# Performance work log

Measured on AMD Instinct MI355X. Metric: run time of the kernel, lower is better.

The kernel has to match this reference:

```python
import jax, jax.numpy as jnp
import numpy as np
from jax import lax

SIZE = 64
N_SUPPORT = 8192
N_QUERIES = 16384
UNROLLING_STEPS = 10


def setup_inputs() -> dict:
    key = jax.random.key(0)
    ks = jax.random.split(key, 6)
    s = 1.0 / np.sqrt(SIZE)
    return {
        "support": jax.random.normal(ks[0], (N_SUPPORT, SIZE), jnp.float32),
        "queries": jax.random.normal(ks[1], (N_QUERIES, SIZE), jnp.float32),
        "W_ih": jax.random.normal(ks[2], (4 * SIZE, SIZE), jnp.float32) * s,
        "W_hh": jax.random.normal(ks[3], (4 * SIZE, SIZE), jnp.float32) * s,
        "b_ih": jax.random.normal(ks[4], (4 * SIZE,), jnp.float32) * s,
        "b_hh": jax.random.normal(ks[5], (4 * SIZE,), jnp.float32) * s,
    }


def _lstm_cell(x, h, c, W_ih, W_hh, b_ih, b_hh):
    # PyTorch LSTMCell gate order: i, f, g, o
    gates = x @ W_ih.T + b_ih + h @ W_hh.T + b_hh  # [B, 4*size]
    i, f, g, o = jnp.split(gates, 4, axis=1)
    c_new = jax.nn.sigmoid(f) * c + jax.nn.sigmoid(i) * jnp.tanh(g)
    h_new = jax.nn.sigmoid(o) * jnp.tanh(c_new)
    return h_new, c_new


def reference(support, queries, W_ih, W_hh, b_ih, b_hh):
    def step(carry, _):
        h_hat, c = carry
        h = h_hat + queries                              # [B, size]
        att = jax.nn.softmax(h @ support.T, axis=1)      # [B, n_support]
        readout = att @ support                          # [B, size]
        h_hat2, c2 = _lstm_cell(queries, h + readout, c, W_ih, W_hh, b_ih, b_hh)
        return (h_hat2, c2), None

    init = (jnp.zeros_like(queries), jnp.zeros_like(queries))
    (h_hat, _), _ = lax.scan(step, init, None, length=UNROLLING_STEPS)
    return h_hat + queries
```

## Files before the change

### kernel.cpp

```cpp
#include <hip/hip_runtime.h>

using u16 = unsigned short;
using u32 = unsigned int;

#define NS 8192
#define NQ 16384
#define SZ 64
#define STEPS 10
#define TS 64
#define TSZ (TS * SZ)
#define NT (NS / TS)
#define NR (NT / 2)
#define L2E 1.44269504088896340736f

typedef __attribute__((ext_vector_type(8))) _Float16 f16x8;
typedef __attribute__((ext_vector_type(4))) float f32x4;

static __device__ __forceinline__ float ex2(float x) { float r; asm("v_exp_f32 %0, %1" : "=v"(r) : "v"(x)); return r; }
static __device__ __forceinline__ float rcp_(float x) { float r; asm("v_rcp_f32 %0, %1" : "=v"(r) : "v"(x)); return r; }

static __device__ __forceinline__ u16 hbits(_Float16 h) { union { _Float16 h; u16 u; } c; c.h = h; return c.u; }
static __device__ __forceinline__ u32 pk2(float lo, float hi) {
    return (u32)hbits((_Float16)lo) | ((u32)hbits((_Float16)hi) << 16);
}
static __device__ __forceinline__ f32x4 MMH(f16x8 a, f16x8 b, f32x4 c) {
    return __builtin_amdgcn_mfma_f32_16x16x32_f16(a, b, c, 0, 0, 0);
}
static __device__ __forceinline__ f16x8 LD(const void* p) { return *(const f16x8*)p; }
static __device__ __forceinline__ float sig(float x) { return rcp_(1.f + ex2(-L2E * x)); }
static __device__ __forceinline__ float tanh_(float x) {
    float e = ex2(-2.f * L2E * x);
    return (1.f - e) * rcp_(1.f + e);
}
static __device__ __forceinline__ void lds_fence() {
    asm volatile("s_waitcnt lgkmcnt(0)" ::: "memory");
    __builtin_amdgcn_sched_barrier(0);
}
static __device__ __forceinline__ void gload16(const void* g, void* l) {
    __builtin_amdgcn_global_load_lds(
        (const __attribute__((address_space(1))) void*)g,
        (__attribute__((address_space(3))) void*)l, 16, 0, 0);
}

__global__ void prep_kernel(const float* __restrict__ sup,
                            const float* __restrict__ Wih,
                            const float* __restrict__ Whh,
                            const float* __restrict__ bih,
                            const float* __restrict__ bhh,
                            u16* __restrict__ supH, u16* __restrict__ supL,
                            u16* __restrict__ supT,
                            u16* __restrict__ WiH, u16* __restrict__ WiL,
                            u16* __restrict__ WhH, u16* __restrict__ WhL,
                            float* __restrict__ bs) {
    int i = blockIdx.x * 256 + threadIdx.x;
    if (i < NS * SZ) {
        float v = sup[i];
        _Float16 hi = (_Float16)v;
        _Float16 lo = (_Float16)(v - (float)hi);
        supH[i] = hbits(hi);
        supL[i] = hbits(lo);
        int s = i >> 6, d = i & 63;
        supT[(s >> 6) * TSZ + d * TS + (s & 63)] = hbits(hi);
    }
    if (i < 4 * SZ * SZ) {
        float a = Wih[i]; _Float16 ah = (_Float16)a;
        WiH[i] = hbits(ah); WiL[i] = hbits((_Float16)(a - (float)ah));
        float b = Whh[i]; _Float16 bh = (_Float16)b;
        WhH[i] = hbits(bh); WhL[i] = hbits((_Float16)(b - (float)bh));
    }
    if (i < 4 * SZ) bs[i] = bih[i] + bhh[i];
}

__global__ __launch_bounds__(1024, 4) void attlstm_kernel(
    const float* __restrict__ queries,
    const u16* __restrict__ supH, const u16* __restrict__ supL,
    const u16* __restrict__ supT,
    const u16* __restrict__ WiH, const u16* __restrict__ WiL,
    const u16* __restrict__ WhH, const u16* __restrict__ WhL,
    const float* __restrict__ bsum,
    float* __restrict__ out) {
    __shared__ __align__(16) u16 stage[4][3][TSZ];
    __shared__ __align__(16) u32 P_lds[16][512];
    __shared__ __align__(16) u16 hsl[4][2048];
    __shared__ __align__(16) float bs_lds[256];

    const int tid = threadIdx.x;
    const int w = tid >> 6;
    const int l = tid & 63;
    const int qg = w & 3;
    const int quarter = w >> 2;
    const int tsel = quarter >> 1;
    const int shalf = quarter & 1;
    const bool lead = (quarter == 0);
    const int q = l & 15;
    const int g = l >> 4;
    const int qrow = blockIdx.x * 64 + qg * 16 + q;
    const u32 swz = (u32)(q & 7) << 4;

    if (tid < 256) bs_lds[tid] = bsum[tid];

    const u16* gsrc[3]; int inoff[3]; int ctsel[3];
#pragma unroll
    for (int j = 0; j < 3; ++j) {
        int c = w + 16 * j;
        ctsel[j] = c / 24;
        int rem = c - 24 * ctsel[j];
        int a = rem >> 3, s8 = rem & 7;
        int srcoff = (s8 * 8 + (l >> 3)) * SZ + ((l & 7) ^ (l >> 3)) * 8;
        gsrc[j] = ((a == 0) ? supH : (a == 1) ? supL : supT) + srcoff;
        inoff[j] = a * TSZ + s8 * 512;
    }
    u16* stg = &stage[0][0][0];
    char* hslb = (char*)&hsl[qg][0];
    char* pw = (char*)&P_lds[w][0];

    float qv[16], hh[16], cc[16];
    f16x8 qfh0, qfh1, qfl0, qfl1;
    if (lead) {
#pragma unroll
        for (int s4 = 0; s4 < 4; ++s4) {
            f32x4 v = *(const f32x4*)&queries[qrow * SZ + 16 * s4 + 4 * g];
#pragma unroll
            for (int jj = 0; jj < 4; ++jj) {
                qv[4 * s4 + jj] = v[jj];
                hh[4 * s4 + jj] = 0.f;
                cc[4 * s4 + jj] = 0.f;
            }
            _Float16 c0 = (_Float16)v[0], c1 = (_Float16)v[1], c2 = (_Float16)v[2], c3 = (_Float16)v[3];
            uint2 whi, wlo;
            whi.x = (u32)hbits(c0) | ((u32)hbits(c1) << 16);
            whi.y = (u32)hbits(c2) | ((u32)hbits(c3) << 16);
            wlo.x = pk2(v[0] - (float)c0, v[1] - (float)c1);
            wlo.y = pk2(v[2] - (float)c2, v[3] - (float)c3);
            u32 b = q * 128 + ((32u * s4 + 8u * g) ^ swz);
            *(uint2*)(hslb + b) = whi;
            *(uint2*)(hslb + 2048 + b) = wlo;
        }
        lds_fence();
        qfh0 = LD(hslb + q * 128 + ((16u * g) ^ swz));
        qfh1 = LD(hslb + q * 128 + ((16u * g + 64u) ^ swz));
        qfl0 = LD(hslb + 2048 + q * 128 + ((16u * g) ^ swz));
        qfl1 = LD(hslb + 2048 + q * 128 + ((16u * g + 64u) ^ swz));
    }

#pragma unroll 1
    for (int step = 0; step < STEPS; ++step) {
        if (lead) {
#pragma unroll
            for (int s4 = 0; s4 < 4; ++s4) {
                float h0 = hh[4 * s4 + 0] + qv[4 * s4 + 0];
                float h1 = hh[4 * s4 + 1] + qv[4 * s4 + 1];
                float h2 = hh[4 * s4 + 2] + qv[4 * s4 + 2];
                float h3 = hh[4 * s4 + 3] + qv[4 * s4 + 3];
                _Float16 a0 = (_Float16)h0, a1 = (_Float16)h1, a2 = (_Float16)h2, a3 = (_Float16)h3;
                uint2 whi, wlo;
                whi.x = (u32)hbits(a0) | ((u32)hbits(a1) << 16);
                whi.y = (u32)hbits(a2) | ((u32)hbits(a3) << 16);
                wlo.x = pk2(h0 - (float)a0, h1 - (float)a1);
                wlo.y = pk2(h2 - (float)a2, h3 - (float)a3);
                u32 b = q * 128 + ((32u * s4 + 8u * g) ^ swz);
                *(uint2*)(hslb + b) = whi;
                *(uint2*)(hslb + 2048 + b) = wlo;
            }
        }
        __syncthreads();
        const f16x8 bh0 = LD(hslb + q * 128 + ((16u * g) ^ swz));
        const f16x8 bh1 = LD(hslb + q * 128 + ((16u * g + 64u) ^ swz));
        const f16x8 bl0 = LD(hslb + 2048 + q * 128 + ((16u * g) ^ swz));
        const f16x8 bl1 = LD(hslb + 2048 + q * 128 + ((16u * g + 64u) ^ swz));

#pragma unroll
        for (int j = 0; j < 3; ++j)
            gload16(gsrc[j] + ctsel[j] * TSZ, stg + ctsel[j] * 12288 + inoff[j]);
        __syncthreads();

        float m = -1e30f, mL = -1.5e30f, lsum = 0.f;
        f32x4 Oa[4] = {{0, 0, 0, 0}, {0, 0, 0, 0}, {0, 0, 0, 0}, {0, 0, 0, 0}};

#pragma unroll 1
        for (int r = 0; r < NR; ++r) {
            if (r < NR - 1) {
#pragma unroll
                for (int j = 0; j < 3; ++j) {
                    int t = 2 * r + 2 + ctsel[j];
                    gload16(gsrc[j] + t * TSZ, stg + (t & 3) * 12288 + inoff[j]);
                }
            }
            const int myslot = (2 * r + tsel) & 3;
            const char* sH = (const char*)(stg + myslot * 12288);
            const char* sL = sH + TSZ * 2;
            const char* sT = sH + 2 * TSZ * 2;
            f32x4 sv[2];
#pragma unroll
            for (int sub = 0; sub < 2; ++sub) {
                u32 rb = (u32)(16 * (2 * shalf + sub) + q) * 128;
                f16x8 aH0 = LD(sH + rb + ((16u * g) ^ swz));
                f16x8 aH1 = LD(sH + rb + ((16u * g + 64u) ^ swz));
                f16x8 aL0 = LD(sL + rb + ((16u * g) ^ swz));
                f16x8 aL1 = LD(sL + rb + ((16u * g + 64u) ^ swz));
                f32x4 a = {0, 0, 0, 0};
                a = MMH(aH0, bh0, a); a = MMH(aH1, bh1, a);
                a = MMH(aH0, bl0, a); a = MMH(aH1, bl1, a);
                a = MMH(aL0, bh0, a); a = MMH(aL1, bh1, a);
                sv[sub] = a;
            }
            float tm = fmaxf(fmaxf(fmaxf(sv[0][0], sv[0][1]), fmaxf(sv[0][2], sv[0][3])),
                             fmaxf(fmaxf(sv[1][0], sv[1][1]), fmaxf(sv[1][2], sv[1][3])));
            tm = fmaxf(tm, __shfl_xor(tm, 16));
            tm = fmaxf(tm, __shfl_xor(tm, 32));
            if (__any(tm > m + 5.5f)) {
                float mn = fmaxf(m, tm);
                float sc = ex2((m - mn) * L2E);
                lsum *= sc;
                Oa[0] *= sc; Oa[1] *= sc; Oa[2] *= sc; Oa[3] *= sc;
                m = mn; mL = m * L2E;
            }
#pragma unroll
            for (int sub = 0; sub < 2; ++sub) {
                float p0 = ex2(sv[sub][0] * L2E - mL);
                float p1 = ex2(sv[sub][1] * L2E - mL);
                float p2 = ex2(sv[sub][2] * L2E - mL);
                float p3 = ex2(sv[sub][3] * L2E - mL);
                lsum += (p0 + p1) + (p2 + p3);
                uint2 wv; wv.x = pk2(p0, p1); wv.y = pk2(p2, p3);
                *(uint2*)(pw + q * 128 + ((32u * sub + 8u * g) ^ swz)) = wv;
            }
            lds_fence();
            f16x8 pb = LD(pw + q * 128 + ((16u * g) ^ swz));
            u32 kbT = (16u * g + 64u * shalf) ^ swz;
#pragma unroll
            for (int dsub = 0; dsub < 4; ++dsub) {
                f16x8 aT = LD(sT + (u32)(16 * dsub + q) * 128 + kbT);
                Oa[dsub] = MMH(aT, pb, Oa[dsub]);
            }
            __syncthreads();
        }
        lsum += __shfl_xor(lsum, 16);
        lsum += __shfl_xor(lsum, 32);

        float* mg = (float*)stg;
        float* mine = mg + (u32)(w * 64 + l) * 20;
        *(f32x4*)(mine + 0) = Oa[0];
        *(f32x4*)(mine + 4) = Oa[1];
        *(f32x4*)(mine + 8) = Oa[2];
        *(f32x4*)(mine + 12) = Oa[3];
        mine[16] = m; mine[17] = lsum;
        __syncthreads();

        if (lead) {
#pragma unroll
            for (int k = 1; k < 4; ++k) {
                const float* oth = mg + (u32)((w + 4 * k) * 64 + l) * 20;
                f32x4 Ob0 = *(const f32x4*)(oth + 0);
                f32x4 Ob1 = *(const f32x4*)(oth + 4);
                f32x4 Ob2 = *(const f32x4*)(oth + 8);
                f32x4 Ob3 = *(const f32x4*)(oth + 12);
                float mo = oth[16], lo_ = oth[17];
                float M = fmaxf(m, mo);
                float sA = ex2((m - M) * L2E), sB = ex2((mo - M) * L2E);
                lsum = lsum * sA + lo_ * sB;
                Oa[0] = Oa[0] * sA + Ob0 * sB;
                Oa[1] = Oa[1] * sA + Ob1 * sB;
                Oa[2] = Oa[2] * sA + Ob2 * sB;
                Oa[3] = Oa[3] * sA + Ob3 * sB;
                m = M;
            }
            float inv = rcp_(lsum);

#pragma unroll
            for (int s4 = 0; s4 < 4; ++s4) {
                float r0 = hh[4 * s4 + 0] + qv[4 * s4 + 0] + Oa[s4][0] * inv;
                float r1 = hh[4 * s4 + 1] + qv[4 * s4 + 1] + Oa[s4][1] * inv;
                float r2 = hh[4 * s4 + 2] + qv[4 * s4 + 2] + Oa[s4][2] * inv;
                float r3 = hh[4 * s4 + 3] + qv[4 * s4 + 3] + Oa[s4][3] * inv;
                _Float16 a0 = (_Float16)r0, a1 = (_Float16)r1, a2 = (_Float16)r2, a3 = (_Float16)r3;
                uint2 whi, wlo;
                whi.x = (u32)hbits(a0) | ((u32)hbits(a1) << 16);
                whi.y = (u32)hbits(a2) | ((u32)hbits(a3) << 16);
                wlo.x = pk2(r0 - (float)a0, r1 - (float)a1);
                wlo.y = pk2(r2 - (float)a2, r3 - (float)a3);
                u32 b = q * 128 + ((32u * s4 + 8u * g) ^ swz);
                *(uint2*)(hslb + b) = whi;
                *(uint2*)(hslb + 2048 + b) = wlo;
            }
            lds_fence();
            const f16x8 rh0 = LD(hslb + q * 128 + ((16u * g) ^ swz));
            const f16x8 rh1 = LD(hslb + q * 128 + ((16u * g + 64u) ^ swz));
            const f16x8 rl0 = LD(hslb + 2048 + q * 128 + ((16u * g) ^ swz));
            const f16x8 rl1 = LD(hslb + 2048 + q * 128 + ((16u * g + 64u) ^ swz));

#pragma unroll
            for (int s4 = 0; s4 < 4; ++s4) {
                f32x4 ga[4];
#pragma unroll
                for (int ch = 0; ch < 4; ++ch) {
                    int u_ = 4 * ch + s4;
                    f32x4 a = *(const f32x4*)&bs_lds[16 * u_ + 4 * g];
                    const u16* wiH = WiH + (16 * u_ + q) * SZ + 8 * g;
                    const u16* wiL = WiL + (16 * u_ + q) * SZ + 8 * g;
                    const u16* whH = WhH + (16 * u_ + q) * SZ + 8 * g;
                    const u16* whL = WhL + (16 * u_ + q) * SZ + 8 * g;
                    f16x8 w0 = LD(wiH), w1 = LD(wiH + 32);
                    a = MMH(w0, qfh0, a); a = MMH(w1, qfh1, a);
                    a = MMH(w0, qfl0, a); a = MMH(w1, qfl1, a);
                    a = MMH(LD(wiL), qfh0, a); a = MMH(LD(wiL + 32), qfh1, a);
                    f16x8 v0 = LD(whH), v1 = LD(whH + 32);
                    a = MMH(v0, rh0, a); a = MMH(v1, rh1, a);
                    a = MMH(v0, rl0, a); a = MMH(v1, rl1, a);
                    a = MMH(LD(whL), rh0, a); a = MMH(LD(whL + 32), rh1, a);
                    ga[ch] = a;
                }
#pragma unroll
                for (int jj = 0; jj < 4; ++jj) {
                    int tt = 4 * s4 + jj;
                    float gi = sig(ga[0][jj]);
                    float gf = sig(ga[1][jj]);
                    float gg = tanh_(ga[2][jj]);
                    float go = sig(ga[3][jj]);
                    float cn = gf * cc[tt] + gi * gg;
                    cc[tt] = cn;
                    hh[tt] = go * tanh_(cn);
                }
            }
        }
    }

    if (lead) {
#pragma unroll
        for (int s4 = 0; s4 < 4; ++s4) {
            f32x4 v;
#pragma unroll
            for (int jj = 0; jj < 4; ++jj) v[jj] = hh[4 * s4 + jj] + qv[4 * s4 + jj];
            *(f32x4*)&out[qrow * SZ + 16 * s4 + 4 * g] = v;
        }
    }
}

extern "C" void kernel_launch(void* const* d_in, const int* in_sizes, int n_in,
                              void* d_out, int out_size, void* d_ws, size_t ws_size,
                              hipStream_t stream) {
    const float* support = (const float*)d_in[0];
    const float* queries = (const float*)d_in[1];
    const float* W_ih = (const float*)d_in[2];
    const float* W_hh = (const float*)d_in[3];
    const float* b_ih = (const float*)d_in[4];
    const float* b_hh = (const float*)d_in[5];
    float* out = (float*)d_out;

    u16* supH = (u16*)d_ws;
    u16* supL = supH + NS * SZ;
    u16* supT = supL + NS * SZ;
    u16* WiH = supT + NS * SZ;
    u16* WiL = WiH + 4 * SZ * SZ;
    u16* WhH = WiL + 4 * SZ * SZ;
    u16* WhL = WhH + 4 * SZ * SZ;
    float* bs = (float*)(WhL + 4 * SZ * SZ);

    prep_kernel<<<(NS * SZ) / 256, 256, 0, stream>>>(support, W_ih, W_hh, b_ih, b_hh,
                                                     supH, supL, supT, WiH, WiL, WhH, WhL, bs);
    attlstm_kernel<<<NQ / 64, 1024, 0, stream>>>(queries, supH, supL, supT,
                                                 WiH, WiL, WhH, WhL, bs, out);
}
```

Measured before the change: 1.460 ms.

## Distribute softmax merge and LSTM cell across all waves instead of lead waves

Before, only the 4 lead waves (quarter 0) did the cross-wave softmax merge, the h/readout conversion and the full LSTM gate matmuls while 12 waves idled. Now every wave handles one 16-column slice (its quarter) of h, c and the gates: each merges the 4 partial attention results for its slice, writes its slice to LDS, and computes one quarter of the gate MFMAs. This shrinks the serial per-step epilogue and per-thread state, at the cost of extra __syncthreads barriers. The launch_bounds occupancy hint is also dropped.

```diff
diff --git a/kernel.cpp b/kernel.cpp
--- a/kernel.cpp
+++ b/kernel.cpp
@@ -71,7 +71,7 @@
     if (i < 4 * SZ) bs[i] = bih[i] + bhh[i];
 }
 
-__global__ __launch_bounds__(1024, 4) void attlstm_kernel(
+__global__ __launch_bounds__(1024) void attlstm_kernel(
     const float* __restrict__ queries,
     const u16* __restrict__ supH, const u16* __restrict__ supL,
     const u16* __restrict__ supT,
@@ -91,11 +91,11 @@
     const int quarter = w >> 2;
     const int tsel = quarter >> 1;
     const int shalf = quarter & 1;
-    const bool lead = (quarter == 0);
     const int q = l & 15;
     const int g = l >> 4;
     const int qrow = blockIdx.x * 64 + qg * 16 + q;
     const u32 swz = (u32)(q & 7) << 4;
+    const u32 bsl = (u32)q * 128 + ((32u * (u32)quarter + 8u * (u32)g) ^ swz);
 
     if (tid < 256) bs_lds[tid] = bsum[tid];
 
@@ -114,54 +114,39 @@
     char* hslb = (char*)&hsl[qg][0];
     char* pw = (char*)&P_lds[w][0];
 
-    float qv[16], hh[16], cc[16];
-    f16x8 qfh0, qfh1, qfl0, qfl1;
-    if (lead) {
-#pragma unroll
-        for (int s4 = 0; s4 < 4; ++s4) {
-            f32x4 v = *(const f32x4*)&queries[qrow * SZ + 16 * s4 + 4 * g];
-#pragma unroll
-            for (int jj = 0; jj < 4; ++jj) {
-                qv[4 * s4 + jj] = v[jj];
-                hh[4 * s4 + jj] = 0.f;
-                cc[4 * s4 + jj] = 0.f;
-            }
-            _Float16 c0 = (_Float16)v[0], c1 = (_Float16)v[1], c2 = (_Float16)v[2], c3 = (_Float16)v[3];
-            uint2 whi, wlo;
-            whi.x = (u32)hbits(c0) | ((u32)hbits(c1) << 16);
-            whi.y = (u32)hbits(c2) | ((u32)hbits(c3) << 16);
-            wlo.x = pk2(v[0] - (float)c0, v[1] - (float)c1);
-            wlo.y = pk2(v[2] - (float)c2, v[3] - (float)c3);
-            u32 b = q * 128 + ((32u * s4 + 8u * g) ^ swz);
-            *(uint2*)(hslb + b) = whi;
-            *(uint2*)(hslb + 2048 + b) = wlo;
-        }
-        lds_fence();
-        qfh0 = LD(hslb + q * 128 + ((16u * g) ^ swz));
-        qfh1 = LD(hslb + q * 128 + ((16u * g + 64u) ^ swz));
-        qfl0 = LD(hslb + 2048 + q * 128 + ((16u * g) ^ swz));
-        qfl1 = LD(hslb + 2048 + q * 128 + ((16u * g + 64u) ^ swz));
-    }
+    float qv[4], hh[4], cc[4];
+    {
+        f32x4 v = *(const f32x4*)&queries[qrow * SZ + 16 * quarter + 4 * g];
+#pragma unroll
+        for (int jj = 0; jj < 4; ++jj) { qv[jj] = v[jj]; hh[jj] = 0.f; cc[jj] = 0.f; }
+        _Float16 c0 = (_Float16)v[0], c1 = (_Float16)v[1], c2 = (_Float16)v[2], c3 = (_Float16)v[3];
+        uint2 whi, wlo;
+        whi.x = (u32)hbits(c0) | ((u32)hbits(c1) << 16);
+        whi.y = (u32)hbits(c2) | ((u32)hbits(c3) << 16);
+        wlo.x = pk2(v[0] - (float)c0, v[1] - (float)c1);
+        wlo.y = pk2(v[2] - (float)c2, v[3] - (float)c3);
+        *(uint2*)(hslb + bsl) = whi;
+        *(uint2*)(hslb + 2048 + bsl) = wlo;
+    }
+    __syncthreads();
+    const f16x8 qfh0 = LD(hslb + q * 128 + ((16u * g) ^ swz));
+    const f16x8 qfh1 = LD(hslb + q * 128 + ((16u * g + 64u) ^ swz));
+    const f16x8 qfl0 = LD(hslb + 2048 + q * 128 + ((16u * g) ^ swz));
+    const f16x8 qfl1 = LD(hslb + 2048 + q * 128 + ((16u * g + 64u) ^ swz));
 
 #pragma unroll 1
     for (int step = 0; step < STEPS; ++step) {
-        if (lead) {
-#pragma unroll
-            for (int s4 = 0; s4 < 4; ++s4) {
-                float h0 = hh[4 * s4 + 0] + qv[4 * s4 + 0];
-                float h1 = hh[4 * s4 + 1] + qv[4 * s4 + 1];
-                float h2 = hh[4 * s4 + 2] + qv[4 * s4 + 2];
-                float h3 = hh[4 * s4 + 3] + qv[4 * s4 + 3];
-                _Float16 a0 = (_Float16)h0, a1 = (_Float16)h1, a2 = (_Float16)h2, a3 = (_Float16)h3;
-                uint2 whi, wlo;
-                whi.x = (u32)hbits(a0) | ((u32)hbits(a1) << 16);
-                whi.y = (u32)hbits(a2) | ((u32)hbits(a3) << 16);
-                wlo.x = pk2(h0 - (float)a0, h1 - (float)a1);
-                wlo.y = pk2(h2 - (float)a2, h3 - (float)a3);
-                u32 b = q * 128 + ((32u * s4 + 8u * g) ^ swz);
-                *(uint2*)(hslb + b) = whi;
-                *(uint2*)(hslb + 2048 + b) = wlo;
-            }
+        __syncthreads();
+        {
+            float h0 = hh[0] + qv[0], h1 = hh[1] + qv[1], h2 = hh[2] + qv[2], h3 = hh[3] + qv[3];
+            _Float16 a0 = (_Float16)h0, a1 = (_Float16)h1, a2 = (_Float16)h2, a3 = (_Float16)h3;
+            uint2 whi, wlo;
+            whi.x = (u32)hbits(a0) | ((u32)hbits(a1) << 16);
+            whi.y = (u32)hbits(a2) | ((u32)hbits(a3) << 16);
+            wlo.x = pk2(h0 - (float)a0, h1 - (float)a1);
+            wlo.y = pk2(h2 - (float)a2, h3 - (float)a3);
+            *(uint2*)(hslb + bsl) = whi;
+            *(uint2*)(hslb + 2048 + bsl) = wlo;
         }
         __syncthreads();
         const f16x8 bh0 = LD(hslb + q * 128 + ((16u * g) ^ swz));
@@ -247,92 +232,81 @@
         mine[16] = m; mine[17] = lsum;
         __syncthreads();
 
-        if (lead) {
-#pragma unroll
-            for (int k = 1; k < 4; ++k) {
-                const float* oth = mg + (u32)((w + 4 * k) * 64 + l) * 20;
-                f32x4 Ob0 = *(const f32x4*)(oth + 0);
-                f32x4 Ob1 = *(const f32x4*)(oth + 4);
-                f32x4 Ob2 = *(const f32x4*)(oth + 8);
-                f32x4 Ob3 = *(const f32x4*)(oth + 12);
-                float mo = oth[16], lo_ = oth[17];
-                float M = fmaxf(m, mo);
-                float sA = ex2((m - M) * L2E), sB = ex2((mo - M) * L2E);
-                lsum = lsum * sA + lo_ * sB;
-                Oa[0] = Oa[0] * sA + Ob0 * sB;
-                Oa[1] = Oa[1] * sA + Ob1 * sB;
-                Oa[2] = Oa[2] * sA + Ob2 * sB;
-                Oa[3] = Oa[3] * sA + Ob3 * sB;
-                m = M;
-            }
-            float inv = rcp_(lsum);
-
-#pragma unroll
-            for (int s4 = 0; s4 < 4; ++s4) {
-                float r0 = hh[4 * s4 + 0] + qv[4 * s4 + 0] + Oa[s4][0] * inv;
-                float r1 = hh[4 * s4 + 1] + qv[4 * s4 + 1] + Oa[s4][1] * inv;
-                float r2 = hh[4 * s4 + 2] + qv[4 * s4 + 2] + Oa[s4][2] * inv;
-                float r3 = hh[4 * s4 + 3] + qv[4 * s4 + 3] + Oa[s4][3] * inv;
-                _Float16 a0 = (_Float16)r0, a1 = (_Float16)r1, a2 = (_Float16)r2, a3 = (_Float16)r3;
-                uint2 whi, wlo;
-                whi.x = (u32)hbits(a0) | ((u32)hbits(a1) << 16);
-                whi.y = (u32)hbits(a2) | ((u32)hbits(a3) << 16);
-                wlo.x = pk2(r0 - (float)a0, r1 - (float)a1);
-                wlo.y = pk2(r2 - (float)a2, r3 - (float)a3);
-                u32 b = q * 128 + ((32u * s4 + 8u * g) ^ swz);
-                *(uint2*)(hslb + b) = whi;
-                *(uint2*)(hslb + 2048 + b) = wlo;
-            }
-            lds_fence();
-            const f16x8 rh0 = LD(hslb + q * 128 + ((16u * g) ^ swz));
-            const f16x8 rh1 = LD(hslb + q * 128 + ((16u * g + 64u) ^ swz));
-            const f16x8 rl0 = LD(hslb + 2048 + q * 128 + ((16u * g) ^ swz));
-            const f16x8 rl1 = LD(hslb + 2048 + q * 128 + ((16u * g + 64u) ^ swz));
-
-#pragma unroll
-            for (int s4 = 0; s4 < 4; ++s4) {
-                f32x4 ga[4];
-#pragma unroll
-                for (int ch = 0; ch < 4; ++ch) {
-                    int u_ = 4 * ch + s4;
-                    f32x4 a = *(const f32x4*)&bs_lds[16 * u_ + 4 * g];
-                    const u16* wiH = WiH + (16 * u_ + q) * SZ + 8 * g;
-                    const u16* wiL = WiL + (16 * u_ + q) * SZ + 8 * g;
-                    const u16* whH = WhH + (16 * u_ + q) * SZ + 8 * g;
-                    const u16* whL = WhL + (16 * u_ + q) * SZ + 8 * g;
-                    f16x8 w0 = LD(wiH), w1 = LD(wiH + 32);
-                    a = MMH(w0, qfh0, a); a = MMH(w1, qfh1, a);
-                    a = MMH(w0, qfl0, a); a = MMH(w1, qfl1, a);
-                    a = MMH(LD(wiL), qfh0, a); a = MMH(LD(wiL + 32), qfh1, a);
-                    f16x8 v0 = LD(whH), v1 = LD(whH + 32);
-                    a = MMH(v0, rh0, a); a = MMH(v1, rh1, a);
-                    a = MMH(v0, rl0, a); a = MMH(v1, rl1, a);
-                    a = MMH(LD(whL), rh0, a); a = MMH(LD(whL + 32), rh1, a);
-                    ga[ch] = a;
-                }
-#pragma unroll
-                for (int jj = 0; jj < 4; ++jj) {
-                    int tt = 4 * s4 + jj;
-                    float gi = sig(ga[0][jj]);
-                    float gf = sig(ga[1][jj]);
-                    float gg = tanh_(ga[2][jj]);
-                    float go = sig(ga[3][jj]);
-                    float cn = gf * cc[tt] + gi * gg;
-                    cc[tt] = cn;
-                    hh[tt] = go * tanh_(cn);
-                }
-            }
-        }
-    }
-
-    if (lead) {
-#pragma unroll
-        for (int s4 = 0; s4 < 4; ++s4) {
-            f32x4 v;
-#pragma unroll
-            for (int jj = 0; jj < 4; ++jj) v[jj] = hh[4 * s4 + jj] + qv[4 * s4 + jj];
-            *(f32x4*)&out[qrow * SZ + 16 * s4 + 4 * g] = v;
-        }
+        float mk[4], lk[4];
+        f32x4 Ok[4];
+#pragma unroll
+        for (int k = 0; k < 4; ++k) {
+            const float* oth = mg + (u32)((qg + 4 * k) * 64 + l) * 20;
+            Ok[k] = *(const f32x4*)(oth + 4 * quarter);
+            mk[k] = oth[16]; lk[k] = oth[17];
+        }
+        float M = fmaxf(fmaxf(mk[0], mk[1]), fmaxf(mk[2], mk[3]));
+        f32x4 Op = {0, 0, 0, 0};
+        float ls = 0.f;
+#pragma unroll
+        for (int k = 0; k < 4; ++k) {
+            float sk = ex2((mk[k] - M) * L2E);
+            ls += lk[k] * sk;
+            Op += Ok[k] * sk;
+        }
+        float inv = rcp_(ls);
+
+        {
+            float r0 = hh[0] + qv[0] + Op[0] * inv;
+            float r1 = hh[1] + qv[1] + Op[1] * inv;
+            float r2 = hh[2] + qv[2] + Op[2] * inv;
+            float r3 = hh[3] + qv[3] + Op[3] * inv;
+            _Float16 a0 = (_Float16)r0, a1 = (_Float16)r1, a2 = (_Float16)r2, a3 = (_Float16)r3;
+            uint2 whi, wlo;
+            whi.x = (u32)hbits(a0) | ((u32)hbits(a1) << 16);
+            whi.y = (u32)hbits(a2) | ((u32)hbits(a3) << 16);
+            wlo.x = pk2(r0 - (float)a0, r1 - (float)a1);
+            wlo.y = pk2(r2 - (float)a2, r3 - (float)a3);
+            *(uint2*)(hslb + bsl) = whi;
+            *(uint2*)(hslb + 2048 + bsl) = wlo;
+        }
+        __syncthreads();
+        const f16x8 rh0 = LD(hslb + q * 128 + ((16u * g) ^ swz));
+        const f16x8 rh1 = LD(hslb + q * 128 + ((16u * g + 64u) ^ swz));
+        const f16x8 rl0 = LD(hslb + 2048 + q * 128 + ((16u * g) ^ swz));
+        const f16x8 rl1 = LD(hslb + 2048 + q * 128 + ((16u * g + 64u) ^ swz));
+
+        f32x4 ga[4];
+#pragma unroll
+        for (int ch = 0; ch < 4; ++ch) {
+            int u_ = 4 * ch + quarter;
+            f32x4 a = *(const f32x4*)&bs_lds[16 * u_ + 4 * g];
+            const u16* wiH = WiH + (16 * u_ + q) * SZ + 8 * g;
+            const u16* wiL = WiL + (16 * u_ + q) * SZ + 8 * g;
+            const u16* whH = WhH + (16 * u_ + q) * SZ + 8 * g;
+            const u16* whL = WhL + (16 * u_ + q) * SZ + 8 * g;
+            f16x8 w0 = LD(wiH), w1 = LD(wiH + 32);
+            a = MMH(w0, qfh0, a); a = MMH(w1, qfh1, a);
+            a = MMH(w0, qfl0, a); a = MMH(w1, qfl1, a);
+            a = MMH(LD(wiL), qfh0, a); a = MMH(LD(wiL + 32), qfh1, a);
+            f16x8 v0 = LD(whH), v1 = LD(whH + 32);
+            a = MMH(v0, rh0, a); a = MMH(v1, rh1, a);
+            a = MMH(v0, rl0, a); a = MMH(v1, rl1, a);
+            a = MMH(LD(whL), rh0, a); a = MMH(LD(whL + 32), rh1, a);
+            ga[ch] = a;
+        }
+#pragma unroll
+        for (int jj = 0; jj < 4; ++jj) {
+            float gi = sig(ga[0][jj]);
+            float gf = sig(ga[1][jj]);
+            float gg = tanh_(ga[2][jj]);
+            float go = sig(ga[3][jj]);
+            float cn = gf * cc[jj] + gi * gg;
+            cc[jj] = cn;
+            hh[jj] = go * tanh_(cn);
+        }
+    }
+
+    {
+        f32x4 v;
+#pragma unroll
+        for (int jj = 0; jj < 4; ++jj) v[jj] = hh[jj] + qv[jj];
+        *(f32x4*)&out[qrow * SZ + 16 * quarter + 4 * g] = v;
     }
 }
 
```

Result: faster. 1.316 ms (-9.9%).
